# Optimization experiments

Hardware: AMD Instinct MI355X
Metric: run time of the kernel (lower is better)

Reference implementation:

```python
import jax, jax.numpy as jnp
import numpy as np
import math

N_HEAD = 9
N_KV_HEAD = 3
HEAD_DIM = 64
ROPE_THETA = 100000.0


def _rope_cos_sin(seq_len, dim, theta):
    inv_freq = 1.0 / (theta ** (jnp.arange(0, dim, 2, dtype=jnp.float32) / dim))  # (dim//2,)
    t = jnp.arange(seq_len, dtype=jnp.float32)
    ang = jnp.outer(t, inv_freq)  # (T, dim//2)
    return jnp.cos(ang), jnp.sin(ang)


def _apply_rope(x, cos, sin):
    # x: (B, H, T, D); pairs are interleaved along D (torch view_as_complex on (..., D//2, 2))
    B, H, T, D = x.shape
    xr = x.reshape(B, H, T, D // 2, 2)
    x0, x1 = xr[..., 0], xr[..., 1]
    c = cos[None, None, :, :]
    s = sin[None, None, :, :]
    out0 = x0 * c - x1 * s
    out1 = x0 * s + x1 * c
    return jnp.stack([out0, out1], axis=-1).reshape(B, H, T, D)


def setup_inputs() -> dict:
    key = jax.random.key(0)
    ks = jax.random.split(key, 5)
    B, T, C = 4, 2048, 576
    scale_in = 1.0 / math.sqrt(C)
    return {
        "x": jax.random.normal(ks[0], (B, T, C), dtype=jnp.float32),
        "wq": jax.random.normal(ks[1], (N_HEAD * HEAD_DIM, C), dtype=jnp.float32) * scale_in,
        "wk": jax.random.normal(ks[2], (N_KV_HEAD * HEAD_DIM, C), dtype=jnp.float32) * scale_in,
        "wv": jax.random.normal(ks[3], (N_KV_HEAD * HEAD_DIM, C), dtype=jnp.float32) * scale_in,
        "wo": jax.random.normal(ks[4], (C, N_HEAD * HEAD_DIM), dtype=jnp.float32) * scale_in,
    }


def reference(x, wq, wk, wv, wo):
    B, T, C = x.shape
    n_rep = N_HEAD // N_KV_HEAD

    q = (x @ wq.T).reshape(B, T, N_HEAD, HEAD_DIM).transpose(0, 2, 1, 3)      # (B,Hq,T,D)
    k = (x @ wk.T).reshape(B, T, N_KV_HEAD, HEAD_DIM).transpose(0, 2, 1, 3)   # (B,Hkv,T,D)
    v = (x @ wv.T).reshape(B, T, N_KV_HEAD, HEAD_DIM).transpose(0, 2, 1, 3)

    cos, sin = _rope_cos_sin(T, HEAD_DIM, ROPE_THETA)
    q = _apply_rope(q, cos, sin)
    k = _apply_rope(k, cos, sin)

    # GQA: broadcast each KV head across n_rep query heads without materializing copies
    qg = q.reshape(B, N_KV_HEAD, n_rep, T, HEAD_DIM)
    att = jnp.einsum("bgrtd,bgsd->bgrts", qg, k) * (1.0 / math.sqrt(HEAD_DIM))  # (B,Hkv,rep,T,T)
    causal = jnp.tril(jnp.ones((T, T), dtype=bool))
    att = jnp.where(causal[None, None, None, :, :], att, -jnp.inf)
    att = jax.nn.softmax(att, axis=-1)
    y = jnp.einsum("bgrts,bgsd->bgrtd", att, v)                                # (B,Hkv,rep,T,D)
    y = y.reshape(B, N_HEAD, T, HEAD_DIM).transpose(0, 2, 1, 3).reshape(B, T, N_HEAD * HEAD_DIM)
    return y @ wo.T
```

## Files before the change

### kernel.cpp

```cpp
#include <hip/hip_runtime.h>
#include <stdint.h>

typedef __attribute__((ext_vector_type(8))) short bf16x8;
typedef __attribute__((ext_vector_type(16))) float f32x16;

#define MFMA32(a, b, c) __builtin_amdgcn_mfma_f32_32x32x16_bf16(a, b, c, 0, 0, 0)

#define BB 4
#define TT 2048
#define CC 576
#define NH 9
#define NKV 3
#define HD 64
#define MM (BB * TT)
#define NQKV 960

#define QSC 0.18033688011112042f

__device__ __forceinline__ unsigned short f2bf(float f) {
  union { float f; uint32_t u; } v; v.f = f;
  uint32_t u = v.u;
  uint32_t r = (u + 0x7fffu + ((u >> 16) & 1u)) >> 16;
  return (unsigned short)r;
}

__device__ __forceinline__ void gl16(const void* g, void* l) {
  __builtin_amdgcn_global_load_lds(
      (const __attribute__((address_space(1))) unsigned int*)g,
      (__attribute__((address_space(3))) unsigned int*)l, 16, 0, 0);
}

__device__ __forceinline__ float fexp2(float x) {
  float r;
  asm("v_exp_f32 %0, %1" : "=v"(r) : "v"(x));
  return r;
}

__global__ __launch_bounds__(256) void prep_kernel(
    const float* __restrict__ x, const float* __restrict__ wq,
    const float* __restrict__ wk, const float* __restrict__ wv,
    const float* __restrict__ wo,
    unsigned short* __restrict__ xh, unsigned short* __restrict__ wqkv,
    unsigned short* __restrict__ woh, float* __restrict__ tc,
    float* __restrict__ ts) {
  const int NX4 = MM * CC / 4;
  const int NW4 = NQKV * CC / 4;
  const int NO4 = CC * CC / 4;
  const int NT = TT * 32;
  const int total = NX4 + NW4 + NO4 + NT;
  for (int i = blockIdx.x * blockDim.x + threadIdx.x; i < total;
       i += gridDim.x * blockDim.x) {
    if (i < NX4) {
      float4 v = ((const float4*)x)[i];
      ushort4 o;
      o.x = f2bf(v.x); o.y = f2bf(v.y); o.z = f2bf(v.z); o.w = f2bf(v.w);
      ((ushort4*)xh)[i] = o;
    } else if (i < NX4 + NW4) {
      int j = i - NX4;
      int n = (j * 4) / CC;
      const float* src = (n < 576) ? wq + j * 4
                       : (n < 768) ? wk + j * 4 - 576 * CC
                                   : wv + j * 4 - 768 * CC;
      float4 v = *(const float4*)src;
      ushort4 o;
      o.x = f2bf(v.x); o.y = f2bf(v.y); o.z = f2bf(v.z); o.w = f2bf(v.w);
      ((ushort4*)wqkv)[j] = o;
    } else if (i < NX4 + NW4 + NO4) {
      int j = i - NX4 - NW4;
      float4 v = ((const float4*)wo)[j];
      ushort4 o;
      o.x = f2bf(v.x); o.y = f2bf(v.y); o.z = f2bf(v.z); o.w = f2bf(v.w);
      ((ushort4*)woh)[j] = o;
    } else {
      int j = i - NX4 - NW4 - NO4;
      int t = j >> 5, pi = j & 31;
      double invf = pow(100000.0, -(double)(2 * pi) / 64.0);
      double ang = (double)t * invf;
      tc[j] = (float)cos(ang);
      ts[j] = (float)sin(ang);
    }
  }
}

__global__ __launch_bounds__(512, 4) void gemm_qkv(
    const unsigned short* __restrict__ xh, const unsigned short* __restrict__ wqkv,
    const float* __restrict__ tc, const float* __restrict__ ts,
    unsigned short* __restrict__ qb, unsigned short* __restrict__ kst,
    unsigned short* __restrict__ vst) {
  const int l = threadIdx.x & 63, w = threadIdx.x >> 6;
  const int ln = l & 31, hi = l >> 5;
  const int bm = blockIdx.y * 256, bn = blockIdx.x * 64;

  __shared__ unsigned short als[2][16384];
  __shared__ unsigned short bls[2][4096];

  int asrc[4];
#pragma unroll
  for (int i = 0; i < 4; ++i)
    asrc[i] = (bm + w * 32 + i * 8 + (l >> 3)) * CC + ((l & 7) ^ ((l >> 3) & 7)) * 8;
  const int bsrc = (bn + w * 8 + (l >> 3)) * CC + ((l & 7) ^ ((l >> 3) & 7)) * 8;

  f32x16 acc0, acc1;
#pragma unroll
  for (int r = 0; r < 16; ++r) { acc0[r] = 0.f; acc1[r] = 0.f; }

#pragma unroll
  for (int i = 0; i < 4; ++i) gl16(xh + asrc[i], (char*)&als[0][0] + w * 4096 + i * 1024);
  gl16(wqkv + bsrc, (char*)&bls[0][0] + w * 1024);

  int cur = 0;
  for (int t = 0; t < 9; ++t) {
    if (t + 1 < 9) {
      const int k0 = (t + 1) * 64;
#pragma unroll
      for (int i = 0; i < 4; ++i)
        gl16(xh + asrc[i] + k0, (char*)&als[cur ^ 1][0] + w * 4096 + i * 1024);
      gl16(wqkv + bsrc + k0, (char*)&bls[cur ^ 1][0] + w * 1024);
      asm volatile("s_waitcnt vmcnt(5)" ::: "memory");
    } else {
      asm volatile("s_waitcnt vmcnt(0)" ::: "memory");
    }
    __builtin_amdgcn_s_barrier();
    __builtin_amdgcn_sched_barrier(0);

    const char* ab = (const char*)&als[cur][0];
    const char* bb = (const char*)&bls[cur][0];
    __builtin_amdgcn_s_setprio(1);
#pragma unroll
    for (int ks = 0; ks < 4; ++ks) {
      const int ch = (((ks * 2 + hi) ^ (ln & 7)) << 4);
      bf16x8 af = *(const bf16x8*)(ab + (w * 32 + ln) * 128 + ch);
      bf16x8 b0 = *(const bf16x8*)(bb + ln * 128 + ch);
      bf16x8 b1 = *(const bf16x8*)(bb + (32 + ln) * 128 + ch);
      acc0 = MFMA32(af, b0, acc0);
      acc1 = MFMA32(af, b1, acc1);
    }
    __builtin_amdgcn_s_setprio(0);

    __builtin_amdgcn_sched_barrier(0);
    __builtin_amdgcn_s_barrier();
    cur ^= 1;
  }

#pragma unroll
  for (int n32 = 0; n32 < 2; ++n32) {
    const int col = bn + n32 * 32 + ln;
    const int d = col & 63;
#pragma unroll
    for (int r = 0; r < 16; ++r) {
      const int m = bm + w * 32 + (r & 3) + 8 * (r >> 2) + 4 * hi;
      float v = n32 ? acc1[r] : acc0[r];
      float partner = __shfl_xor(v, 1);
      const int bi = m >> 11, t = m & 2047;
      if (col < 768) {
        const int pi = d >> 1;
        const float c = tc[t * 32 + pi], s = ts[t * 32 + pi];
        v = (d & 1) ? (partner * s + v * c) : (v * c - partner * s);
      }
      if (col < 576) {
        const int h = col >> 6;
        qb[(((size_t)bi * NH + h) * TT + t) * HD + d] = f2bf(v * QSC);
      } else if (col < 768) {
        const int h = (col - 576) >> 6;
        const size_t head = (size_t)bi * NKV + h;
        kst[((head * 32 + (t >> 6)) * 64 + (t & 63)) * 64 + (d ^ ((t & 7) << 3))] = f2bf(v);
      } else {
        const int h = (col - 768) >> 6;
        const size_t head = (size_t)bi * NKV + h;
        vst[((head * 32 + (t >> 6)) * 64 + d) * 64 + ((t & 63) ^ ((d & 7) << 3))] = f2bf(v);
      }
    }
  }
}

__global__ __launch_bounds__(512, 2) void attn_kernel(
    const unsigned short* __restrict__ qbuf, const unsigned short* __restrict__ kst,
    const unsigned short* __restrict__ vst, unsigned short* __restrict__ yb) {
  const int j = blockIdx.x, kvh = blockIdx.y, b = blockIdx.z;
  const int i = j & 3, hr = j >> 2;
  const int h = kvh * 3 + hr;
  const int l = threadIdx.x & 63;
  const int w8 = threadIdx.x >> 6;
  const int g = w8 >> 2;
  const int wq = w8 & 3;
  const int ln = l & 31, hi = l >> 5;
  const size_t head = (size_t)b * NKV + kvh;

  const int qt0 = 7 - i, qt1 = i;
  const int m0 = 2 * qt0 + 2, m1 = 2 * qt1 + 2;
  const int tot = m0 + m1;

  __shared__ unsigned short kls[2][3][4096];
  __shared__ unsigned short vls[2][3][4096];
  __shared__ float licomb[256];

  const unsigned short* qptr = qbuf + ((size_t)b * NH + h) * TT * HD;

  int qrA = qt0 * 256 + wq * 64 + ln;
  bf16x8 qa[4], qb_[4];
#pragma unroll
  for (int ds = 0; ds < 4; ++ds) {
    qa[ds]  = *(const bf16x8*)(qptr + (size_t)qrA * HD + ds * 16 + hi * 8);
    qb_[ds] = *(const bf16x8*)(qptr + (size_t)(qrA + 32) * HD + ds * 16 + hi * 8);
  }
  int qt_c = qt0, nt_c = m0;

  const char* kgb = (const char*)(kst + head * 32 * 4096);
  const char* vgb = (const char*)(vst + head * 32 * 4096);

  f32x16 oA0, oA1, oB0, oB1, fzero;
  float lsA[4], lsB[4];
#pragma unroll
  for (int r = 0; r < 16; ++r) { oA0[r] = 0.f; oA1[r] = 0.f; oB0[r] = 0.f; oB1[r] = 0.f; fzero[r] = 0.f; }
#pragma unroll
  for (int r = 0; r < 4; ++r) { lsA[r] = 0.f; lsB[r] = 0.f; }

#pragma unroll
  for (int pre = 0; pre < 2; ++pre) {
    const size_t tb = (size_t)(2 * pre + g) * 8192;
#pragma unroll
    for (int i2 = 0; i2 < 2; ++i2) {
      const int off = wq * 2048 + i2 * 1024;
      gl16(kgb + tb + off + l * 16, (char*)&kls[g][pre][0] + off);
      gl16(vgb + tb + off + l * 16, (char*)&vls[g][pre][0] + off);
    }
  }
  asm volatile("s_waitcnt vmcnt(4)" ::: "memory");
  __builtin_amdgcn_s_barrier();
  __builtin_amdgcn_sched_barrier(0);

  const int swz = (ln & 7) << 4;
  int jt = 0;

  for (int it = 0; it < tot; ++it) {
    if (it + 2 < tot) {
      const int f = it + 2;
      const int u2 = (f < m0) ? f : f - m0;
      const size_t tb = (size_t)(2 * u2 + g) * 8192;
      char* kl = (char*)&kls[g][(it + 2) % 3][0];
      char* vl = (char*)&vls[g][(it + 2) % 3][0];
#pragma unroll
      for (int i2 = 0; i2 < 2; ++i2) {
        const int off = wq * 2048 + i2 * 1024;
        gl16(kgb + tb + off + l * 16, kl + off);
        gl16(vgb + tb + off + l * 16, vl + off);
      }
    }

    const char* kb = (const char*)&kls[g][it % 3][0];
    const char* vb = (const char*)&vls[g][it % 3][0];
    const int kvt = 2 * jt + g;

    f32x16 sA0, sA1, sB0, sB1;
    __builtin_amdgcn_s_setprio(1);
    {
      const int cb0 = (hi * 16) ^ swz;
      bf16x8 k0 = *(const bf16x8*)(kb + ln * 128 + cb0);
      bf16x8 k1 = *(const bf16x8*)(kb + (32 + ln) * 128 + cb0);
      sA0 = MFMA32(k0, qa[0], fzero);
      sB0 = MFMA32(k0, qb_[0], fzero);
      sA1 = MFMA32(k1, qa[0], fzero);
      sB1 = MFMA32(k1, qb_[0], fzero);
    }
#pragma unroll
    for (int ds = 1; ds < 4; ++ds) {
      const int cb = (ds * 32 + hi * 16) ^ swz;
      bf16x8 k0 = *(const bf16x8*)(kb + ln * 128 + cb);
      bf16x8 k1 = *(const bf16x8*)(kb + (32 + ln) * 128 + cb);
      sA0 = MFMA32(k0, qa[ds], sA0);
      sB0 = MFMA32(k0, qb_[ds], sB0);
      sA1 = MFMA32(k1, qa[ds], sA1);
      sB1 = MFMA32(k1, qb_[ds], sB1);
    }
    __builtin_amdgcn_s_setprio(0);

    if (jt >= nt_c - 2) {
#pragma unroll
      for (int r = 0; r < 16; ++r) {
        const int kg = kvt * 64 + (r & 3) + 8 * (r >> 2) + 4 * hi;
        if (kg > qrA) sA0[r] = -1e30f;
        if (kg + 32 > qrA) sA1[r] = -1e30f;
        if (kg > qrA + 32) sB0[r] = -1e30f;
        if (kg + 32 > qrA + 32) sB1[r] = -1e30f;
      }
    }

#pragma unroll
    for (int r = 0; r < 16; ++r) {
      sA0[r] = fexp2(sA0[r]); sA1[r] = fexp2(sA1[r]);
      sB0[r] = fexp2(sB0[r]); sB1[r] = fexp2(sB1[r]);
    }
#pragma unroll
    for (int r = 0; r < 16; ++r) {
      lsA[r & 3] += sA0[r] + sA1[r];
      lsB[r & 3] += sB0[r] + sB1[r];
    }

    unsigned int paA[4][4], paB[4][4];
#pragma unroll
    for (int t = 0; t < 2; ++t) {
#pragma unroll
      for (int m = 0; m < 2; ++m) {
        {
          float p0 = t ? sA1[8 * m + 0] : sA0[8 * m + 0];
          float p1 = t ? sA1[8 * m + 1] : sA0[8 * m + 1];
          float p2 = t ? sA1[8 * m + 2] : sA0[8 * m + 2];
          float p3 = t ? sA1[8 * m + 3] : sA0[8 * m + 3];
          float p4 = t ? sA1[8 * m + 4] : sA0[8 * m + 4];
          float p5 = t ? sA1[8 * m + 5] : sA0[8 * m + 5];
          float p6 = t ? sA1[8 * m + 6] : sA0[8 * m + 6];
          float p7 = t ? sA1[8 * m + 7] : sA0[8 * m + 7];
          unsigned int w0, w1, w2, w3;
          asm("v_cvt_pk_bf16_f32 %0, %1, %2" : "=v"(w0) : "v"(p0), "v"(p1));
          asm("v_cvt_pk_bf16_f32 %0, %1, %2" : "=v"(w1) : "v"(p2), "v"(p3));
          asm("v_cvt_pk_bf16_f32 %0, %1, %2" : "=v"(w2) : "v"(p4), "v"(p5));
          asm("v_cvt_pk_bf16_f32 %0, %1, %2" : "=v"(w3) : "v"(p6), "v"(p7));
          asm("v_permlane32_swap_b32 %0, %1" : "+v"(w0), "+v"(w2));
          asm("v_permlane32_swap_b32 %0, %1" : "+v"(w1), "+v"(w3));
          paA[2 * t + m][0] = w0; paA[2 * t + m][1] = w1;
          paA[2 * t + m][2] = w2; paA[2 * t + m][3] = w3;
        }
        {
          float p0 = t ? sB1[8 * m + 0] : sB0[8 * m + 0];
          float p1 = t ? sB1[8 * m + 1] : sB0[8 * m + 1];
          float p2 = t ? sB1[8 * m + 2] : sB0[8 * m + 2];
          float p3 = t ? sB1[8 * m + 3] : sB0[8 * m + 3];
          float p4 = t ? sB1[8 * m + 4] : sB0[8 * m + 4];
          float p5 = t ? sB1[8 * m + 5] : sB0[8 * m + 5];
          float p6 = t ? sB1[8 * m + 6] : sB0[8 * m + 6];
          float p7 = t ? sB1[8 * m + 7] : sB0[8 * m + 7];
          unsigned int w0, w1, w2, w3;
          asm("v_cvt_pk_bf16_f32 %0, %1, %2" : "=v"(w0) : "v"(p0), "v"(p1));
          asm("v_cvt_pk_bf16_f32 %0, %1, %2" : "=v"(w1) : "v"(p2), "v"(p3));
          asm("v_cvt_pk_bf16_f32 %0, %1, %2" : "=v"(w2) : "v"(p4), "v"(p5));
          asm("v_cvt_pk_bf16_f32 %0, %1, %2" : "=v"(w3) : "v"(p6), "v"(p7));
          asm("v_permlane32_swap_b32 %0, %1" : "+v"(w0), "+v"(w2));
          asm("v_permlane32_swap_b32 %0, %1" : "+v"(w1), "+v"(w3));
          paB[2 * t + m][0] = w0; paB[2 * t + m][1] = w1;
          paB[2 * t + m][2] = w2; paB[2 * t + m][3] = w3;
        }
      }
    }

    __builtin_amdgcn_s_setprio(1);
#pragma unroll
    for (int ks = 0; ks < 4; ++ks) {
      union { unsigned int u[4]; bf16x8 v; } ca, cb2;
      ca.u[0] = paA[ks][0]; ca.u[1] = paA[ks][1];
      ca.u[2] = paA[ks][2]; ca.u[3] = paA[ks][3];
      cb2.u[0] = paB[ks][0]; cb2.u[1] = paB[ks][1];
      cb2.u[2] = paB[ks][2]; cb2.u[3] = paB[ks][3];
      const int cb = (ks * 32 + hi * 16) ^ swz;
      bf16x8 v0 = *(const bf16x8*)(vb + ln * 128 + cb);
      bf16x8 v1 = *(const bf16x8*)(vb + (32 + ln) * 128 + cb);
      oA0 = MFMA32(ca.v, v0, oA0);
      oB0 = MFMA32(cb2.v, v0, oB0);
      oA1 = MFMA32(ca.v, v1, oA1);
      oB1 = MFMA32(cb2.v, v1, oB1);
    }
    __builtin_amdgcn_s_setprio(0);

    if (jt == nt_c - 1) {
      float lA = (lsA[0] + lsA[1]) + (lsA[2] + lsA[3]);
      lA += __shfl_xor(lA, 32);
      float lB = (lsB[0] + lsB[1]) + (lsB[2] + lsB[3]);
      lB += __shfl_xor(lB, 32);
      const int buf = it % 3;
      char* chunk = (char*)((wq == 0) ? &kls[0][buf][0]
                   : (wq == 1) ? &vls[0][buf][0]
                   : (wq == 2) ? &kls[1][buf][0]
                               : &vls[1][buf][0]);
      __builtin_amdgcn_sched_barrier(0);
      __builtin_amdgcn_s_barrier();
      if (g == 1) {
#pragma unroll
        for (int r = 0; r < 16; ++r) {
          *(float*)(chunk + r * 256 + l * 4) = oA0[r];
          *(float*)(chunk + (16 + r) * 256 + l * 4) = oA1[r];
        }
        licomb[wq * 64 + l] = lA;
      }
      asm volatile("s_waitcnt lgkmcnt(0)" ::: "memory");
      __builtin_amdgcn_s_barrier();
      if (g == 0) {
#pragma unroll
        for (int r = 0; r < 16; ++r) {
          oA0[r] += *(const float*)(chunk + r * 256 + l * 4);
          oA1[r] += *(const float*)(chunk + (16 + r) * 256 + l * 4);
        }
        const float inv = 1.0f / (lA + licomb[wq * 64 + l]);
#pragma unroll
        for (int r = 0; r < 16; ++r) {
          const int cr = (r & 3) + 8 * (r >> 2) + 4 * hi;
          const float ir = __shfl(inv, cr);
          const int t = qt_c * 256 + wq * 64 + cr;
          unsigned short* yp = yb + ((size_t)b * TT + t) * CC + h * HD;
          yp[ln] = f2bf(oA0[r] * ir);
          yp[32 + ln] = f2bf(oA1[r] * ir);
        }
      }
      __builtin_amdgcn_s_barrier();
      if (g == 1) {
#pragma unroll
        for (int r = 0; r < 16; ++r) {
          *(float*)(chunk + r * 256 + l * 4) = oB0[r];
          *(float*)(chunk + (16 + r) * 256 + l * 4) = oB1[r];
        }
        licomb[wq * 64 + l] = lB;
      }
      asm volatile("s_waitcnt lgkmcnt(0)" ::: "memory");
      __builtin_amdgcn_s_barrier();
      if (g == 0) {
#pragma unroll
        for (int r = 0; r < 16; ++r) {
          oB0[r] += *(const float*)(chunk + r * 256 + l * 4);
          oB1[r] += *(const float*)(chunk + (16 + r) * 256 + l * 4);
        }
        const float inv = 1.0f / (lB + licomb[wq * 64 + l]);
#pragma unroll
        for (int r = 0; r < 16; ++r) {
          const int cr = (r & 3) + 8 * (r >> 2) + 4 * hi;
          const float ir = __shfl(inv, cr);
          const int t = qt_c * 256 + wq * 64 + 32 + cr;
          unsigned short* yp = yb + ((size_t)b * TT + t) * CC + h * HD;
          yp[ln] = f2bf(oB0[r] * ir);
          yp[32 + ln] = f2bf(oB1[r] * ir);
        }
      }
      oA0 = fzero; oA1 = fzero; oB0 = fzero; oB1 = fzero;
#pragma unroll
      for (int r = 0; r < 4; ++r) { lsA[r] = 0.f; lsB[r] = 0.f; }
      if (it + 1 < tot) {
        qt_c = qt1; nt_c = m1;
        qrA = qt1 * 256 + wq * 64 + ln;
#pragma unroll
        for (int ds = 0; ds < 4; ++ds) {
          qa[ds]  = *(const bf16x8*)(qptr + (size_t)qrA * HD + ds * 16 + hi * 8);
          qb_[ds] = *(const bf16x8*)(qptr + (size_t)(qrA + 32) * HD + ds * 16 + hi * 8);
        }
        jt = -1;
      }
    }

    __builtin_amdgcn_sched_barrier(0);
    if (it + 2 < tot) {
      asm volatile("s_waitcnt vmcnt(4)" ::: "memory");
    } else {
      asm volatile("s_waitcnt vmcnt(0)" ::: "memory");
    }
    __builtin_amdgcn_s_barrier();
    __builtin_amdgcn_sched_barrier(0);
    ++jt;
  }
}

__global__ __launch_bounds__(512, 4) void gemm_out(
    const unsigned short* __restrict__ yb, const unsigned short* __restrict__ woh,
    float* __restrict__ out) {
  const int l = threadIdx.x & 63, w = threadIdx.x >> 6;
  const int ln = l & 31, hi = l >> 5;
  const int bm = blockIdx.y * 256, bn = blockIdx.x * 64;

  __shared__ unsigned short als[2][16384];
  __shared__ unsigned short bls[2][4096];

  int asrc[4];
#pragma unroll
  for (int i = 0; i < 4; ++i)
    asrc[i] = (bm + w * 32 + i * 8 + (l >> 3)) * CC + ((l & 7) ^ ((l >> 3) & 7)) * 8;
  const int bsrc = (bn + w * 8 + (l >> 3)) * CC + ((l & 7) ^ ((l >> 3) & 7)) * 8;

  f32x16 acc0, acc1;
#pragma unroll
  for (int r = 0; r < 16; ++r) { acc0[r] = 0.f; acc1[r] = 0.f; }

#pragma unroll
  for (int i = 0; i < 4; ++i) gl16(yb + asrc[i], (char*)&als[0][0] + w * 4096 + i * 1024);
  gl16(woh + bsrc, (char*)&bls[0][0] + w * 1024);

  int cur = 0;
  for (int t = 0; t < 9; ++t) {
    if (t + 1 < 9) {
      const int k0 = (t + 1) * 64;
#pragma unroll
      for (int i = 0; i < 4; ++i)
        gl16(yb + asrc[i] + k0, (char*)&als[cur ^ 1][0] + w * 4096 + i * 1024);
      gl16(woh + bsrc + k0, (char*)&bls[cur ^ 1][0] + w * 1024);
      asm volatile("s_waitcnt vmcnt(5)" ::: "memory");
    } else {
      asm volatile("s_waitcnt vmcnt(0)" ::: "memory");
    }
    __builtin_amdgcn_s_barrier();
    __builtin_amdgcn_sched_barrier(0);

    const char* ab = (const char*)&als[cur][0];
    const char* bb = (const char*)&bls[cur][0];
    __builtin_amdgcn_s_setprio(1);
#pragma unroll
    for (int ks = 0; ks < 4; ++ks) {
      const int ch = (((ks * 2 + hi) ^ (ln & 7)) << 4);
      bf16x8 af = *(const bf16x8*)(ab + (w * 32 + ln) * 128 + ch);
      bf16x8 b0 = *(const bf16x8*)(bb + ln * 128 + ch);
      bf16x8 b1 = *(const bf16x8*)(bb + (32 + ln) * 128 + ch);
      acc0 = MFMA32(af, b0, acc0);
      acc1 = MFMA32(af, b1, acc1);
    }
    __builtin_amdgcn_s_setprio(0);

    __builtin_amdgcn_sched_barrier(0);
    __builtin_amdgcn_s_barrier();
    cur ^= 1;
  }

#pragma unroll
  for (int n32 = 0; n32 < 2; ++n32) {
    const int col = bn + n32 * 32 + ln;
#pragma unroll
    for (int r = 0; r < 16; ++r) {
      const int m = bm + w * 32 + (r & 3) + 8 * (r >> 2) + 4 * hi;
      out[(size_t)m * CC + col] = n32 ? acc1[r] : acc0[r];
    }
  }
}

extern "C" void kernel_launch(void* const* d_in, const int* in_sizes, int n_in,
                              void* d_out, int out_size, void* d_ws, size_t ws_size,
                              hipStream_t stream) {
  const float* x = (const float*)d_in[0];
  const float* wq = (const float*)d_in[1];
  const float* wk = (const float*)d_in[2];
  const float* wv = (const float*)d_in[3];
  const float* wo = (const float*)d_in[4];
  float* out = (float*)d_out;

  char* ws = (char*)d_ws;
  unsigned short* xh = (unsigned short*)ws;    ws += (size_t)MM * CC * 2;
  unsigned short* wqkv = (unsigned short*)ws;  ws += (size_t)NQKV * CC * 2;
  unsigned short* woh = (unsigned short*)ws;   ws += (size_t)CC * CC * 2;
  float* tc = (float*)ws;                      ws += (size_t)TT * 32 * 4;
  float* tsn = (float*)ws;                     ws += (size_t)TT * 32 * 4;
  unsigned short* qbuf = (unsigned short*)ws;  ws += (size_t)BB * NH * TT * HD * 2;
  unsigned short* kst = (unsigned short*)ws;   ws += (size_t)BB * NKV * TT * HD * 2;
  unsigned short* vst = (unsigned short*)ws;   ws += (size_t)BB * NKV * HD * TT * 2;
  unsigned short* yb = (unsigned short*)ws;    ws += (size_t)MM * CC * 2;

  prep_kernel<<<dim3(2048), dim3(256), 0, stream>>>(x, wq, wk, wv, wo, xh, wqkv, woh, tc, tsn);
  gemm_qkv<<<dim3(NQKV / 64, MM / 256), dim3(512), 0, stream>>>(xh, wqkv, tc, tsn, qbuf, kst, vst);
  attn_kernel<<<dim3(12, NKV, BB), dim3(512), 0, stream>>>(qbuf, kst, vst, yb);
  gemm_out<<<dim3(CC / 64, MM / 256), dim3(512), 0, stream>>>(yb, woh, out);
}
```

Baseline: 111.2 us.

## Restructure attention into per-64-row query blocks with split-KV waves reading global directly

Result: slower. 192.3 us (+72.9%).

```diff
diff --git a/kernel.cpp b/kernel.cpp
--- a/kernel.cpp
+++ b/kernel.cpp
@@ -163,47 +163,41 @@
       } else if (col < 768) {
         const int h = (col - 576) >> 6;
         const size_t head = (size_t)bi * NKV + h;
-        kst[((head * 32 + (t >> 6)) * 64 + (t & 63)) * 64 + (d ^ ((t & 7) << 3))] = f2bf(v);
+        const int tt = t & 63;
+        kst[(head * 32 + (t >> 6)) * 4096 + ((d >> 4) * 2 + (tt >> 5)) * 512
+            + ((((d >> 3) & 1) << 5) + (tt & 31)) * 8 + (d & 7)] = f2bf(v);
       } else {
         const int h = (col - 768) >> 6;
         const size_t head = (size_t)bi * NKV + h;
-        vst[((head * 32 + (t >> 6)) * 64 + d) * 64 + ((t & 63) ^ ((d & 7) << 3))] = f2bf(v);
+        const int tt = t & 63;
+        vst[(head * 32 + (t >> 6)) * 4096 + ((tt >> 4) * 2 + (d >> 5)) * 512
+            + ((((tt >> 3) & 1) << 5) + (d & 31)) * 8 + (tt & 7)] = f2bf(v);
       }
     }
   }
 }
 
-__global__ __launch_bounds__(512, 2) void attn_kernel(
+__global__ __launch_bounds__(256) void attn_kernel(
     const unsigned short* __restrict__ qbuf, const unsigned short* __restrict__ kst,
     const unsigned short* __restrict__ vst, unsigned short* __restrict__ yb) {
-  const int j = blockIdx.x, kvh = blockIdx.y, b = blockIdx.z;
-  const int i = j & 3, hr = j >> 2;
-  const int h = kvh * 3 + hr;
-  const int l = threadIdx.x & 63;
-  const int w8 = threadIdx.x >> 6;
-  const int g = w8 >> 2;
-  const int wq = w8 & 3;
+  const int qc = 31 - blockIdx.x, h = blockIdx.y, b = blockIdx.z;
+  const int l = threadIdx.x & 63, w = threadIdx.x >> 6;
   const int ln = l & 31, hi = l >> 5;
+  const int kvh = h / 3;
   const size_t head = (size_t)b * NKV + kvh;
 
-  const int qt0 = 7 - i, qt1 = i;
-  const int m0 = 2 * qt0 + 2, m1 = 2 * qt1 + 2;
-  const int tot = m0 + m1;
-
-  __shared__ unsigned short kls[2][3][4096];
-  __shared__ unsigned short vls[2][3][4096];
-  __shared__ float licomb[256];
+  __shared__ float ob[64][64];
+  __shared__ float lb[64];
 
   const unsigned short* qptr = qbuf + ((size_t)b * NH + h) * TT * HD;
-
-  int qrA = qt0 * 256 + wq * 64 + ln;
+  const int qrA = qc * 64 + ln;
+
   bf16x8 qa[4], qb_[4];
 #pragma unroll
   for (int ds = 0; ds < 4; ++ds) {
     qa[ds]  = *(const bf16x8*)(qptr + (size_t)qrA * HD + ds * 16 + hi * 8);
     qb_[ds] = *(const bf16x8*)(qptr + (size_t)(qrA + 32) * HD + ds * 16 + hi * 8);
   }
-  int qt_c = qt0, nt_c = m0;
 
   const char* kgb = (const char*)(kst + head * 32 * 4096);
   const char* vgb = (const char*)(vst + head * 32 * 4096);
@@ -215,69 +209,32 @@
 #pragma unroll
   for (int r = 0; r < 4; ++r) { lsA[r] = 0.f; lsB[r] = 0.f; }
 
-#pragma unroll
-  for (int pre = 0; pre < 2; ++pre) {
-    const size_t tb = (size_t)(2 * pre + g) * 8192;
-#pragma unroll
-    for (int i2 = 0; i2 < 2; ++i2) {
-      const int off = wq * 2048 + i2 * 1024;
-      gl16(kgb + tb + off + l * 16, (char*)&kls[g][pre][0] + off);
-      gl16(vgb + tb + off + l * 16, (char*)&vls[g][pre][0] + off);
-    }
-  }
-  asm volatile("s_waitcnt vmcnt(4)" ::: "memory");
-  __builtin_amdgcn_s_barrier();
-  __builtin_amdgcn_sched_barrier(0);
-
-  const int swz = (ln & 7) << 4;
-  int jt = 0;
-
-  for (int it = 0; it < tot; ++it) {
-    if (it + 2 < tot) {
-      const int f = it + 2;
-      const int u2 = (f < m0) ? f : f - m0;
-      const size_t tb = (size_t)(2 * u2 + g) * 8192;
-      char* kl = (char*)&kls[g][(it + 2) % 3][0];
-      char* vl = (char*)&vls[g][(it + 2) % 3][0];
-#pragma unroll
-      for (int i2 = 0; i2 < 2; ++i2) {
-        const int off = wq * 2048 + i2 * 1024;
-        gl16(kgb + tb + off + l * 16, kl + off);
-        gl16(vgb + tb + off + l * 16, vl + off);
+  for (int j = w; j <= qc; j += 4) {
+    const char* kt = kgb + (size_t)j * 8192;
+    const char* vt = vgb + (size_t)j * 8192;
+
+    f32x16 sA0, sA1, sB0, sB1;
+#pragma unroll
+    for (int ds = 0; ds < 4; ++ds) {
+      bf16x8 k0 = *(const bf16x8*)(kt + (ds * 2 + 0) * 1024 + l * 16);
+      bf16x8 k1 = *(const bf16x8*)(kt + (ds * 2 + 1) * 1024 + l * 16);
+      if (ds == 0) {
+        sA0 = MFMA32(k0, qa[0], fzero);
+        sB0 = MFMA32(k0, qb_[0], fzero);
+        sA1 = MFMA32(k1, qa[0], fzero);
+        sB1 = MFMA32(k1, qb_[0], fzero);
+      } else {
+        sA0 = MFMA32(k0, qa[ds], sA0);
+        sB0 = MFMA32(k0, qb_[ds], sB0);
+        sA1 = MFMA32(k1, qa[ds], sA1);
+        sB1 = MFMA32(k1, qb_[ds], sB1);
       }
     }
 
-    const char* kb = (const char*)&kls[g][it % 3][0];
-    const char* vb = (const char*)&vls[g][it % 3][0];
-    const int kvt = 2 * jt + g;
-
-    f32x16 sA0, sA1, sB0, sB1;
-    __builtin_amdgcn_s_setprio(1);
-    {
-      const int cb0 = (hi * 16) ^ swz;
-      bf16x8 k0 = *(const bf16x8*)(kb + ln * 128 + cb0);
-      bf16x8 k1 = *(const bf16x8*)(kb + (32 + ln) * 128 + cb0);
-      sA0 = MFMA32(k0, qa[0], fzero);
-      sB0 = MFMA32(k0, qb_[0], fzero);
-      sA1 = MFMA32(k1, qa[0], fzero);
-      sB1 = MFMA32(k1, qb_[0], fzero);
-    }
-#pragma unroll
-    for (int ds = 1; ds < 4; ++ds) {
-      const int cb = (ds * 32 + hi * 16) ^ swz;
-      bf16x8 k0 = *(const bf16x8*)(kb + ln * 128 + cb);
-      bf16x8 k1 = *(const bf16x8*)(kb + (32 + ln) * 128 + cb);
-      sA0 = MFMA32(k0, qa[ds], sA0);
-      sB0 = MFMA32(k0, qb_[ds], sB0);
-      sA1 = MFMA32(k1, qa[ds], sA1);
-      sB1 = MFMA32(k1, qb_[ds], sB1);
-    }
-    __builtin_amdgcn_s_setprio(0);
-
-    if (jt >= nt_c - 2) {
+    if (j == qc) {
 #pragma unroll
       for (int r = 0; r < 16; ++r) {
-        const int kg = kvt * 64 + (r & 3) + 8 * (r >> 2) + 4 * hi;
+        const int kg = j * 64 + (r & 3) + 8 * (r >> 2) + 4 * hi;
         if (kg > qrA) sA0[r] = -1e30f;
         if (kg + 32 > qrA) sA1[r] = -1e30f;
         if (kg > qrA + 32) sB0[r] = -1e30f;
@@ -342,7 +299,6 @@
       }
     }
 
-    __builtin_amdgcn_s_setprio(1);
 #pragma unroll
     for (int ks = 0; ks < 4; ++ks) {
       union { unsigned int u[4]; bf16x8 v; } ca, cb2;
@@ -350,107 +306,75 @@
       ca.u[2] = paA[ks][2]; ca.u[3] = paA[ks][3];
       cb2.u[0] = paB[ks][0]; cb2.u[1] = paB[ks][1];
       cb2.u[2] = paB[ks][2]; cb2.u[3] = paB[ks][3];
-      const int cb = (ks * 32 + hi * 16) ^ swz;
-      bf16x8 v0 = *(const bf16x8*)(vb + ln * 128 + cb);
-      bf16x8 v1 = *(const bf16x8*)(vb + (32 + ln) * 128 + cb);
+      bf16x8 v0 = *(const bf16x8*)(vt + (ks * 2 + 0) * 1024 + l * 16);
+      bf16x8 v1 = *(const bf16x8*)(vt + (ks * 2 + 1) * 1024 + l * 16);
       oA0 = MFMA32(ca.v, v0, oA0);
       oB0 = MFMA32(cb2.v, v0, oB0);
       oA1 = MFMA32(ca.v, v1, oA1);
       oB1 = MFMA32(cb2.v, v1, oB1);
     }
-    __builtin_amdgcn_s_setprio(0);
-
-    if (jt == nt_c - 1) {
-      float lA = (lsA[0] + lsA[1]) + (lsA[2] + lsA[3]);
-      lA += __shfl_xor(lA, 32);
-      float lB = (lsB[0] + lsB[1]) + (lsB[2] + lsB[3]);
-      lB += __shfl_xor(lB, 32);
-      const int buf = it % 3;
-      char* chunk = (char*)((wq == 0) ? &kls[0][buf][0]
-                   : (wq == 1) ? &vls[0][buf][0]
-                   : (wq == 2) ? &kls[1][buf][0]
-                               : &vls[1][buf][0]);
-      __builtin_amdgcn_sched_barrier(0);
-      __builtin_amdgcn_s_barrier();
-      if (g == 1) {
-#pragma unroll
-        for (int r = 0; r < 16; ++r) {
-          *(float*)(chunk + r * 256 + l * 4) = oA0[r];
-          *(float*)(chunk + (16 + r) * 256 + l * 4) = oA1[r];
-        }
-        licomb[wq * 64 + l] = lA;
-      }
-      asm volatile("s_waitcnt lgkmcnt(0)" ::: "memory");
-      __builtin_amdgcn_s_barrier();
-      if (g == 0) {
-#pragma unroll
-        for (int r = 0; r < 16; ++r) {
-          oA0[r] += *(const float*)(chunk + r * 256 + l * 4);
-          oA1[r] += *(const float*)(chunk + (16 + r) * 256 + l * 4);
-        }
-        const float inv = 1.0f / (lA + licomb[wq * 64 + l]);
-#pragma unroll
-        for (int r = 0; r < 16; ++r) {
-          const int cr = (r & 3) + 8 * (r >> 2) + 4 * hi;
-          const float ir = __shfl(inv, cr);
-          const int t = qt_c * 256 + wq * 64 + cr;
-          unsigned short* yp = yb + ((size_t)b * TT + t) * CC + h * HD;
-          yp[ln] = f2bf(oA0[r] * ir);
-          yp[32 + ln] = f2bf(oA1[r] * ir);
-        }
-      }
-      __builtin_amdgcn_s_barrier();
-      if (g == 1) {
-#pragma unroll
-        for (int r = 0; r < 16; ++r) {
-          *(float*)(chunk + r * 256 + l * 4) = oB0[r];
-          *(float*)(chunk + (16 + r) * 256 + l * 4) = oB1[r];
-        }
-        licomb[wq * 64 + l] = lB;
-      }
-      asm volatile("s_waitcnt lgkmcnt(0)" ::: "memory");
-      __builtin_amdgcn_s_barrier();
-      if (g == 0) {
-#pragma unroll
-        for (int r = 0; r < 16; ++r) {
-          oB0[r] += *(const float*)(chunk + r * 256 + l * 4);
-          oB1[r] += *(const float*)(chunk + (16 + r) * 256 + l * 4);
-        }
-        const float inv = 1.0f / (lB + licomb[wq * 64 + l]);
-#pragma unroll
-        for (int r = 0; r < 16; ++r) {
-          const int cr = (r & 3) + 8 * (r >> 2) + 4 * hi;
-          const float ir = __shfl(inv, cr);
-          const int t = qt_c * 256 + wq * 64 + 32 + cr;
-          unsigned short* yp = yb + ((size_t)b * TT + t) * CC + h * HD;
-          yp[ln] = f2bf(oB0[r] * ir);
-          yp[32 + ln] = f2bf(oB1[r] * ir);
-        }
-      }
-      oA0 = fzero; oA1 = fzero; oB0 = fzero; oB1 = fzero;
-#pragma unroll
-      for (int r = 0; r < 4; ++r) { lsA[r] = 0.f; lsB[r] = 0.f; }
-      if (it + 1 < tot) {
-        qt_c = qt1; nt_c = m1;
-        qrA = qt1 * 256 + wq * 64 + ln;
-#pragma unroll
-        for (int ds = 0; ds < 4; ++ds) {
-          qa[ds]  = *(const bf16x8*)(qptr + (size_t)qrA * HD + ds * 16 + hi * 8);
-          qb_[ds] = *(const bf16x8*)(qptr + (size_t)(qrA + 32) * HD + ds * 16 + hi * 8);
-        }
-        jt = -1;
-      }
-    }
-
-    __builtin_amdgcn_sched_barrier(0);
-    if (it + 2 < tot) {
-      asm volatile("s_waitcnt vmcnt(4)" ::: "memory");
-    } else {
-      asm volatile("s_waitcnt vmcnt(0)" ::: "memory");
-    }
-    __builtin_amdgcn_s_barrier();
-    __builtin_amdgcn_sched_barrier(0);
-    ++jt;
+  }
+
+  float lA = (lsA[0] + lsA[1]) + (lsA[2] + lsA[3]);
+  lA += __shfl_xor(lA, 32);
+  float lB = (lsB[0] + lsB[1]) + (lsB[2] + lsB[3]);
+  lB += __shfl_xor(lB, 32);
+
+  if (w == 0) {
+#pragma unroll
+    for (int r = 0; r < 16; ++r) {
+      const int cr = (r & 3) + 8 * (r >> 2) + 4 * hi;
+      ob[cr][ln] = oA0[r];
+      ob[cr][32 + ln] = oA1[r];
+      ob[32 + cr][ln] = oB0[r];
+      ob[32 + cr][32 + ln] = oB1[r];
+    }
+    if (hi == 0) { lb[ln] = lA; lb[32 + ln] = lB; }
+  }
+  __syncthreads();
+  if (w == 1) {
+#pragma unroll
+    for (int r = 0; r < 16; ++r) {
+      const int cr = (r & 3) + 8 * (r >> 2) + 4 * hi;
+      ob[cr][ln] += oA0[r];
+      ob[cr][32 + ln] += oA1[r];
+      ob[32 + cr][ln] += oB0[r];
+      ob[32 + cr][32 + ln] += oB1[r];
+    }
+    if (hi == 0) { lb[ln] += lA; lb[32 + ln] += lB; }
+  }
+  __syncthreads();
+  if (w == 2) {
+#pragma unroll
+    for (int r = 0; r < 16; ++r) {
+      const int cr = (r & 3) + 8 * (r >> 2) + 4 * hi;
+      ob[cr][ln] += oA0[r];
+      ob[cr][32 + ln] += oA1[r];
+      ob[32 + cr][ln] += oB0[r];
+      ob[32 + cr][32 + ln] += oB1[r];
+    }
+    if (hi == 0) { lb[ln] += lA; lb[32 + ln] += lB; }
+  }
+  __syncthreads();
+  if (w == 3) {
+#pragma unroll
+    for (int r = 0; r < 16; ++r) {
+      const int cr = (r & 3) + 8 * (r >> 2) + 4 * hi;
+      ob[cr][ln] += oA0[r];
+      ob[cr][32 + ln] += oA1[r];
+      ob[32 + cr][ln] += oB0[r];
+      ob[32 + cr][32 + ln] += oB1[r];
+    }
+    if (hi == 0) { lb[ln] += lA; lb[32 + ln] += lB; }
+  }
+  __syncthreads();
+
+#pragma unroll
+  for (int k = 0; k < 16; ++k) {
+    const int idx = k * 256 + threadIdx.x;
+    const int row = idx >> 6, d = idx & 63;
+    yb[((size_t)b * TT + qc * 64 + row) * CC + h * HD + d] =
+        f2bf(ob[row][d] / lb[row]);
   }
 }
 
@@ -546,6 +470,6 @@
 
   prep_kernel<<<dim3(2048), dim3(256), 0, stream>>>(x, wq, wk, wv, wo, xh, wqkv, woh, tc, tsn);
   gemm_qkv<<<dim3(NQKV / 64, MM / 256), dim3(512), 0, stream>>>(xh, wqkv, tc, tsn, qbuf, kst, vst);
-  attn_kernel<<<dim3(12, NKV, BB), dim3(512), 0, stream>>>(qbuf, kst, vst, yb);
+  attn_kernel<<<dim3(32, NH, BB), dim3(256), 0, stream>>>(qbuf, kst, vst, yb);
   gemm_out<<<dim3(CC / 64, MM / 256), dim3(512), 0, stream>>>(yb, woh, out);
 }
```
